# Performance work log

Hardware: AMD Instinct MI355X
Metric: run time of the kernel (lower is better)

The kernel has to match this reference:

```python
import jax, jax.numpy as jnp
import numpy as np

SIGMA = 1.0


def _rbf_gram(A, B):
    # A: (Tb, N, C), B: (Tb, M, C) -> (Tb, N, M)
    AA = jnp.sum(A * A, axis=2, keepdims=True)          # (Tb, N, 1)
    BB = jnp.sum(B * B, axis=2, keepdims=True)          # (Tb, M, 1)
    d = AA + jnp.swapaxes(BB, 1, 2) - 2.0 * jnp.einsum('bnc,bmc->bnm', A, B)
    return jnp.exp(-d / (2.0 * SIGMA ** 2))


def setup_inputs() -> dict:
    key = jax.random.key(0)
    kx, ky = jax.random.split(key)
    x = jax.random.normal(kx, (512, 128, 16), dtype=jnp.float32)
    y = jax.random.normal(ky, (512, 128, 16), dtype=jnp.float32)
    return {"x": x, "y": y}


def reference(x, y):
    # x, y: (batch, stream, channel)
    x_fds = jnp.concatenate((x[:, :-1, :], x[:, 1:, :]), axis=1)  # (B, 2(T-1), C)
    y_fds = jnp.concatenate((y[:, :-1, :], y[:, 1:, :]), axis=1)
    xf = jnp.transpose(x_fds, (1, 0, 2))  # (2(T-1), B, C)
    yf = jnp.transpose(y_fds, (1, 0, 2))

    N = xf.shape[1]
    Kxx = _rbf_gram(xf, xf)  # (2(T-1), N, N)
    # off-diagonal mean per batch: (sum - trace) / (N*(N-1))
    e_xx = (Kxx.sum(axis=(1, 2)) - jnp.trace(Kxx, axis1=1, axis2=2)) / (N * (N - 1))
    E_k_x1_x2 = e_xx.mean()

    Kxy = _rbf_gram(xf, yf)
    E_k_x_y = Kxy.mean(axis=(1, 2)).mean()

    return E_k_x1_x2 - 2.0 * E_k_x_y
```

## Files before the change

kernel.cpp:

```cpp
#include <hip/hip_runtime.h>


#define LOG2E 1.4426950408889634f
#define SCALE 1.2011224087864498f

typedef __attribute__((ext_vector_type(8))) __bf16 bf16x8;
typedef __attribute__((ext_vector_type(4))) float floatx4;

union FragU { uint4 q; unsigned int u[4]; bf16x8 v; };

static __device__ __forceinline__ int off(int n) { return (n << 3) + ((n >> 2) << 2); }

static __device__ __forceinline__ unsigned short bfbits(__bf16 h) {
    union { __bf16 h; unsigned short s; } u; u.h = h; return u.s;
}
static __device__ __forceinline__ unsigned int packhh(__bf16 a, __bf16 b) {
    return (unsigned int)bfbits(a) | ((unsigned int)bfbits(b) << 16);
}

#define NSLOT 26
#define ONEONE 0x3F803F80u

__global__ __launch_bounds__(256, 8) void mmd_kernel(const float* __restrict__ x,
                                                     const float* __restrict__ y,
                                                     float* __restrict__ part) {
    __shared__ unsigned int AH[1152], BH[1152];
    __shared__ unsigned int BG[512];
    __shared__ float srg[128];
    __shared__ unsigned int zero4[4];
    __shared__ float red[4];

    const int slot = blockIdx.x;
    const int t    = blockIdx.y;
    const int tid  = threadIdx.x;
    const int w    = tid >> 6;
    const int lane = tid & 63;
    const int quad = lane >> 4;
    const int l15  = lane & 15;
    const int qh   = quad & 1;

    int sa, sq, isxx;
    if (slot < 16) { isxx = 0; sa = slot >> 2; sq = slot & 3; }
    else {
        isxx = 1;
        const int s = slot - 16;
        if      (s < 4) { sa = 0; sq = s; }
        else if (s < 7) { sa = 1; sq = s - 3; }
        else if (s < 9) { sa = 2; sq = s - 5; }
        else            { sa = 3; sq = 3; }
    }

    if (tid == 0) { zero4[0] = 0u; zero4[1] = 0u; zero4[2] = 0u; zero4[3] = 0u; }

    {
        const int half = tid >> 7;
        const int r    = tid & 127;
        const int grow = (half ? sq : sa) * 128 + r;
        const float4* __restrict__ src4 =
            (half && !isxx) ? (const float4*)y : (const float4*)x;
        const size_t gb = (size_t)grow * 512 + t * 4;
        float4 f0 = src4[gb], f1 = src4[gb + 1], f2 = src4[gb + 2], f3 = src4[gb + 3];
        const float fs[16] = { f0.x, f0.y, f0.z, f0.w, f1.x, f1.y, f1.z, f1.w,
                               f2.x, f2.y, f2.z, f2.w, f3.x, f3.y, f3.z, f3.w };
        float g = 0.f;
        unsigned int hw[8];
#pragma unroll
        for (int p = 0; p < 8; ++p) {
            const float v0 = fs[2 * p], v1 = fs[2 * p + 1];
            g += v0 * v0 + v1 * v1;
            hw[p] = packhh((__bf16)(v0 * SCALE), (__bf16)(v1 * SCALE));
        }
        const float gp = 0.5f * LOG2E * g;
        unsigned int* __restrict__ H = half ? BH : AH;
        const int o = off(r);
        *(uint4*)&H[o]     = make_uint4(hw[0], hw[1], hw[2], hw[3]);
        *(uint4*)&H[o + 4] = make_uint4(hw[4], hw[5], hw[6], hw[7]);
        if (half) {
            const __bf16 nh = (__bf16)(-gp);
            const __bf16 nl = (__bf16)(-(gp + (float)nh));
            *(uint4*)&BG[r * 4] = make_uint4(packhh(nh, nl), 0u, 0u, 0u);
        } else {
            srg[r] = gp;
        }
    }
    __syncthreads();

    bf16x8 a1f[2];
    {
#pragma unroll
        for (int rt = 0; rt < 2; ++rt) {
            FragU u;
            if (quad < 2) {
                const int row = w * 32 + rt * 16 + l15;
                u.q = *(const uint4*)&AH[off(row) + qh * 4];
            } else {
                u.q = make_uint4((quad == 2) ? ONEONE : 0u, 0u, 0u, 0u);
            }
            a1f[rt] = u.v;
        }
    }

    const unsigned int* bptr;
    int bstride;
    if (quad < 2)      { bptr = &BH[off(l15) + qh * 4]; bstride = 144; }
    else if (quad == 2){ bptr = &BG[l15 * 4];           bstride = 64;  }
    else               { bptr = &zero4[0];              bstride = 0;   }

    float sum[2][4] = {{0.f, 0.f, 0.f, 0.f}, {0.f, 0.f, 0.f, 0.f}};

    floatx4 accP[2], accC[2];
    {
        FragU b; b.q = *(const uint4*)bptr; bptr += bstride;
        floatx4 zc = {0.f, 0.f, 0.f, 0.f};
        accP[0] = __builtin_amdgcn_mfma_f32_16x16x32_bf16(a1f[0], b.v, zc, 0, 0, 0);
        accP[1] = __builtin_amdgcn_mfma_f32_16x16x32_bf16(a1f[1], b.v, zc, 0, 0, 0);
    }
#pragma unroll
    for (int jt = 1; jt < 8; ++jt) {
        FragU b; b.q = *(const uint4*)bptr; bptr += bstride;
        floatx4 zc = {0.f, 0.f, 0.f, 0.f};
        accC[0] = __builtin_amdgcn_mfma_f32_16x16x32_bf16(a1f[0], b.v, zc, 0, 0, 0);
        accC[1] = __builtin_amdgcn_mfma_f32_16x16x32_bf16(a1f[1], b.v, zc, 0, 0, 0);
#pragma unroll
        for (int rt = 0; rt < 2; ++rt)
#pragma unroll
            for (int r = 0; r < 4; ++r)
                sum[rt][r] += __builtin_amdgcn_exp2f(accP[rt][r]);
        accP[0] = accC[0];
        accP[1] = accC[1];
    }
#pragma unroll
    for (int rt = 0; rt < 2; ++rt)
#pragma unroll
        for (int r = 0; r < 4; ++r)
            sum[rt][r] += __builtin_amdgcn_exp2f(accP[rt][r]);

    float tot = 0.f;
#pragma unroll
    for (int rt = 0; rt < 2; ++rt)
#pragma unroll
        for (int r = 0; r < 4; ++r) {
            const float rs = __builtin_amdgcn_exp2f(-srg[w * 32 + rt * 16 + quad * 4 + r]);
            tot = fmaf(sum[rt][r], rs, tot);
        }
    for (int o = 32; o > 0; o >>= 1) tot += __shfl_down(tot, o, 64);
    if (lane == 0) red[w] = tot;
    __syncthreads();
    if (tid == 0) {
        float wt = (t == 0 || t == 127) ? 1.f : 2.f;
        if (isxx && sq > sa) wt *= 2.f;
        const int idx = isxx ? (2048 + t * 10 + (slot - 16)) : (t * 16 + slot);
        part[idx] = wt * (red[0] + red[1] + red[2] + red[3]);
    }
}

__global__ __launch_bounds__(256) void finalize_kernel(const float* __restrict__ part,
                                                       float* __restrict__ out) {
    const int tid = threadIdx.x;
    double vxy = 0.0, vxx = 0.0;
#pragma unroll
    for (int k = 0; k < 8; ++k)  vxy += (double)part[tid + 256 * k];
#pragma unroll
    for (int k = 8; k < 13; ++k) vxx += (double)part[tid + 256 * k];
    for (int o = 32; o > 0; o >>= 1) {
        vxx += __shfl_down(vxx, o, 64);
        vxy += __shfl_down(vxy, o, 64);
    }
    __shared__ double red[8];
    const int wid = tid >> 6;
    if ((tid & 63) == 0) { red[wid] = vxx; red[4 + wid] = vxy; }
    __syncthreads();
    if (tid == 0) {
        double sxx = red[0] + red[1] + red[2] + red[3];
        double sxy = red[4] + red[5] + red[6] + red[7];
        double e1 = (sxx - 254.0 * 512.0) / (254.0 * 512.0 * 511.0);
        double e2 = sxy / (254.0 * 512.0 * 512.0);
        out[0] = (float)(e1 - 2.0 * e2);
    }
}

extern "C" void kernel_launch(void* const* d_in, const int* in_sizes, int n_in,
                              void* d_out, int out_size, void* d_ws, size_t ws_size,
                              hipStream_t stream) {
    (void)in_sizes; (void)n_in; (void)out_size; (void)ws_size;
    const float* x = (const float*)d_in[0];
    const float* y = (const float*)d_in[1];
    float* out  = (float*)d_out;
    float* part = (float*)d_ws;

    mmd_kernel<<<dim3(NSLOT, 128), dim3(256), 0, stream>>>(x, y, part);
    finalize_kernel<<<dim3(1), dim3(256), 0, stream>>>(part, out);
}
```

Before: 71.04 us.

## Process four time steps per block with double-buffered LDS and prefetch

Each block now handles four consecutive time indices instead of one. It double-buffers the bf16 staging in shared memory and prefetches the next step's global loads while the current step's MFMA/exp work runs. Per-wave partial sums are written directly to the workspace, which drops the cross-wave shared reduction, and the finalize kernel reads four times as many partials. The grid shrinks from 3328 to 832 blocks, which amortizes launch and setup cost but reduces parallelism, and launch bounds are relaxed to 4 waves per SIMD.

```diff
diff --git a/kernel.cpp b/kernel.cpp
--- a/kernel.cpp
+++ b/kernel.cpp
@@ -21,17 +21,16 @@
 #define NSLOT 26
 #define ONEONE 0x3F803F80u
 
-__global__ __launch_bounds__(256, 8) void mmd_kernel(const float* __restrict__ x,
+__global__ __launch_bounds__(256, 4) void mmd_kernel(const float* __restrict__ x,
                                                      const float* __restrict__ y,
                                                      float* __restrict__ part) {
-    __shared__ unsigned int AH[1152], BH[1152];
-    __shared__ unsigned int BG[512];
-    __shared__ float srg[128];
+    __shared__ unsigned int AH[2][1152], BH[2][1152];
+    __shared__ unsigned int BG[2][512];
+    __shared__ float srg[2][128];
     __shared__ unsigned int zero4[4];
-    __shared__ float red[4];
 
     const int slot = blockIdx.x;
-    const int t    = blockIdx.y;
+    const int t0   = blockIdx.y << 2;
     const int tid  = threadIdx.x;
     const int w    = tid >> 6;
     const int lane = tid & 63;
@@ -52,16 +51,18 @@
 
     if (tid == 0) { zero4[0] = 0u; zero4[1] = 0u; zero4[2] = 0u; zero4[3] = 0u; }
 
-    {
-        const int half = tid >> 7;
-        const int r    = tid & 127;
-        const int grow = (half ? sq : sa) * 128 + r;
-        const float4* __restrict__ src4 =
-            (half && !isxx) ? (const float4*)y : (const float4*)x;
-        const size_t gb = (size_t)grow * 512 + t * 4;
-        float4 f0 = src4[gb], f1 = src4[gb + 1], f2 = src4[gb + 2], f3 = src4[gb + 3];
-        const float fs[16] = { f0.x, f0.y, f0.z, f0.w, f1.x, f1.y, f1.z, f1.w,
-                               f2.x, f2.y, f2.z, f2.w, f3.x, f3.y, f3.z, f3.w };
+    const int half = tid >> 7;
+    const int r    = tid & 127;
+    const int grow = (half ? sq : sa) * 128 + r;
+    const float4* __restrict__ src4 =
+        (half && !isxx) ? (const float4*)y : (const float4*)x;
+    const size_t gb = (size_t)grow * 512 + (size_t)t0 * 4;
+
+    float4 pf0 = src4[gb], pf1 = src4[gb + 1], pf2 = src4[gb + 2], pf3 = src4[gb + 3];
+
+    auto stage = [&](int b) {
+        const float fs[16] = { pf0.x, pf0.y, pf0.z, pf0.w, pf1.x, pf1.y, pf1.z, pf1.w,
+                               pf2.x, pf2.y, pf2.z, pf2.w, pf3.x, pf3.y, pf3.z, pf3.w };
         float g = 0.f;
         unsigned int hw[8];
 #pragma unroll
@@ -71,86 +72,102 @@
             hw[p] = packhh((__bf16)(v0 * SCALE), (__bf16)(v1 * SCALE));
         }
         const float gp = 0.5f * LOG2E * g;
-        unsigned int* __restrict__ H = half ? BH : AH;
+        unsigned int* __restrict__ H = half ? &BH[b][0] : &AH[b][0];
         const int o = off(r);
         *(uint4*)&H[o]     = make_uint4(hw[0], hw[1], hw[2], hw[3]);
         *(uint4*)&H[o + 4] = make_uint4(hw[4], hw[5], hw[6], hw[7]);
         if (half) {
             const __bf16 nh = (__bf16)(-gp);
             const __bf16 nl = (__bf16)(-(gp + (float)nh));
-            *(uint4*)&BG[r * 4] = make_uint4(packhh(nh, nl), 0u, 0u, 0u);
+            *(uint4*)&BG[b][r * 4] = make_uint4(packhh(nh, nl), 0u, 0u, 0u);
         } else {
-            srg[r] = gp;
-        }
-    }
+            srg[b][r] = gp;
+        }
+    };
+
+    stage(0);
     __syncthreads();
 
-    bf16x8 a1f[2];
-    {
+#pragma unroll
+    for (int u = 0; u < 4; ++u) {
+        const int b = u & 1;
+
+        if (u < 3) {
+            const size_t gu = gb + (size_t)(u + 1) * 4;
+            pf0 = src4[gu]; pf1 = src4[gu + 1]; pf2 = src4[gu + 2]; pf3 = src4[gu + 3];
+        }
+
+        bf16x8 a1f[2];
 #pragma unroll
         for (int rt = 0; rt < 2; ++rt) {
-            FragU u;
+            FragU fu;
             if (quad < 2) {
                 const int row = w * 32 + rt * 16 + l15;
-                u.q = *(const uint4*)&AH[off(row) + qh * 4];
+                fu.q = *(const uint4*)&AH[b][off(row) + qh * 4];
             } else {
-                u.q = make_uint4((quad == 2) ? ONEONE : 0u, 0u, 0u, 0u);
+                fu.q = make_uint4((quad == 2) ? ONEONE : 0u, 0u, 0u, 0u);
             }
-            a1f[rt] = u.v;
-        }
-    }
-
-    const unsigned int* bptr;
-    int bstride;
-    if (quad < 2)      { bptr = &BH[off(l15) + qh * 4]; bstride = 144; }
-    else if (quad == 2){ bptr = &BG[l15 * 4];           bstride = 64;  }
-    else               { bptr = &zero4[0];              bstride = 0;   }
-
-    float sum[2][4] = {{0.f, 0.f, 0.f, 0.f}, {0.f, 0.f, 0.f, 0.f}};
-
-    floatx4 accP[2], accC[2];
-    {
-        FragU b; b.q = *(const uint4*)bptr; bptr += bstride;
-        floatx4 zc = {0.f, 0.f, 0.f, 0.f};
-        accP[0] = __builtin_amdgcn_mfma_f32_16x16x32_bf16(a1f[0], b.v, zc, 0, 0, 0);
-        accP[1] = __builtin_amdgcn_mfma_f32_16x16x32_bf16(a1f[1], b.v, zc, 0, 0, 0);
-    }
-#pragma unroll
-    for (int jt = 1; jt < 8; ++jt) {
-        FragU b; b.q = *(const uint4*)bptr; bptr += bstride;
-        floatx4 zc = {0.f, 0.f, 0.f, 0.f};
-        accC[0] = __builtin_amdgcn_mfma_f32_16x16x32_bf16(a1f[0], b.v, zc, 0, 0, 0);
-        accC[1] = __builtin_amdgcn_mfma_f32_16x16x32_bf16(a1f[1], b.v, zc, 0, 0, 0);
+            a1f[rt] = fu.v;
+        }
+
+        const unsigned int* bptr;
+        int bstride;
+        if (quad < 2)       { bptr = &BH[b][off(l15) + qh * 4]; bstride = 144; }
+        else if (quad == 2) { bptr = &BG[b][l15 * 4];           bstride = 64;  }
+        else                { bptr = &zero4[0];                 bstride = 0;   }
+
+        float sum[2][4] = {{0.f, 0.f, 0.f, 0.f}, {0.f, 0.f, 0.f, 0.f}};
+
+        floatx4 accP[2], accC[2];
+        {
+            FragU bf; bf.q = *(const uint4*)bptr; bptr += bstride;
+            floatx4 zc = {0.f, 0.f, 0.f, 0.f};
+            accP[0] = __builtin_amdgcn_mfma_f32_16x16x32_bf16(a1f[0], bf.v, zc, 0, 0, 0);
+            accP[1] = __builtin_amdgcn_mfma_f32_16x16x32_bf16(a1f[1], bf.v, zc, 0, 0, 0);
+        }
+#pragma unroll
+        for (int jt = 1; jt < 8; ++jt) {
+            FragU bf; bf.q = *(const uint4*)bptr; bptr += bstride;
+            floatx4 zc = {0.f, 0.f, 0.f, 0.f};
+            accC[0] = __builtin_amdgcn_mfma_f32_16x16x32_bf16(a1f[0], bf.v, zc, 0, 0, 0);
+            accC[1] = __builtin_amdgcn_mfma_f32_16x16x32_bf16(a1f[1], bf.v, zc, 0, 0, 0);
+#pragma unroll
+            for (int rt = 0; rt < 2; ++rt)
+#pragma unroll
+                for (int rr = 0; rr < 4; ++rr)
+                    sum[rt][rr] += __builtin_amdgcn_exp2f(accP[rt][rr]);
+            accP[0] = accC[0];
+            accP[1] = accC[1];
+        }
 #pragma unroll
         for (int rt = 0; rt < 2; ++rt)
 #pragma unroll
-            for (int r = 0; r < 4; ++r)
-                sum[rt][r] += __builtin_amdgcn_exp2f(accP[rt][r]);
-        accP[0] = accC[0];
-        accP[1] = accC[1];
-    }
-#pragma unroll
-    for (int rt = 0; rt < 2; ++rt)
-#pragma unroll
-        for (int r = 0; r < 4; ++r)
-            sum[rt][r] += __builtin_amdgcn_exp2f(accP[rt][r]);
-
-    float tot = 0.f;
-#pragma unroll
-    for (int rt = 0; rt < 2; ++rt)
-#pragma unroll
-        for (int r = 0; r < 4; ++r) {
-            const float rs = __builtin_amdgcn_exp2f(-srg[w * 32 + rt * 16 + quad * 4 + r]);
-            tot = fmaf(sum[rt][r], rs, tot);
-        }
-    for (int o = 32; o > 0; o >>= 1) tot += __shfl_down(tot, o, 64);
-    if (lane == 0) red[w] = tot;
-    __syncthreads();
-    if (tid == 0) {
-        float wt = (t == 0 || t == 127) ? 1.f : 2.f;
-        if (isxx && sq > sa) wt *= 2.f;
-        const int idx = isxx ? (2048 + t * 10 + (slot - 16)) : (t * 16 + slot);
-        part[idx] = wt * (red[0] + red[1] + red[2] + red[3]);
+            for (int rr = 0; rr < 4; ++rr)
+                sum[rt][rr] += __builtin_amdgcn_exp2f(accP[rt][rr]);
+
+        float tot = 0.f;
+#pragma unroll
+        for (int rt = 0; rt < 2; ++rt)
+#pragma unroll
+            for (int rr = 0; rr < 4; ++rr) {
+                const float rs =
+                    __builtin_amdgcn_exp2f(-srg[b][w * 32 + rt * 16 + quad * 4 + rr]);
+                tot = fmaf(sum[rt][rr], rs, tot);
+            }
+        for (int o2 = 32; o2 > 0; o2 >>= 1) tot += __shfl_down(tot, o2, 64);
+
+        if (lane == 0) {
+            const int t = t0 + u;
+            float wt = (t == 0 || t == 127) ? 1.f : 2.f;
+            if (isxx && sq > sa) wt *= 2.f;
+            const int idx = isxx ? (2048 + t * 10 + (slot - 16)) : (t * 16 + slot);
+            part[idx * 4 + w] = wt * tot;
+        }
+
+        if (u < 3) {
+            stage(b ^ 1);
+            __syncthreads();
+        }
     }
 }
 
@@ -159,9 +176,9 @@
     const int tid = threadIdx.x;
     double vxy = 0.0, vxx = 0.0;
 #pragma unroll
-    for (int k = 0; k < 8; ++k)  vxy += (double)part[tid + 256 * k];
-#pragma unroll
-    for (int k = 8; k < 13; ++k) vxx += (double)part[tid + 256 * k];
+    for (int k = 0; k < 32; ++k)  vxy += (double)part[tid + 256 * k];
+#pragma unroll
+    for (int k = 32; k < 52; ++k) vxx += (double)part[tid + 256 * k];
     for (int o = 32; o > 0; o >>= 1) {
         vxx += __shfl_down(vxx, o, 64);
         vxy += __shfl_down(vxy, o, 64);
@@ -188,6 +205,6 @@
     float* out  = (float*)d_out;
     float* part = (float*)d_ws;
 
-    mmd_kernel<<<dim3(NSLOT, 128), dim3(256), 0, stream>>>(x, y, part);
+    mmd_kernel<<<dim3(NSLOT, 32), dim3(256), 0, stream>>>(x, y, part);
     finalize_kernel<<<dim3(1), dim3(256), 0, stream>>>(part, out);
 }
```

Result: slower. 76.82 us (+8.1%).
